# Kernel optimization log

Measured on AMD Instinct MI355X. Metric: run time of the kernel, lower is better.

The kernel has to match this reference:

```python
import jax, jax.numpy as jnp
import numpy as np


def _expand_chunk(x):
    # prepend the previous bucket along the chunk axis: [b, nb, bl, ...] -> [b, nb, 2*bl, ...]
    return jnp.concatenate([jnp.roll(x, 1, axis=1), x], axis=2)


def _gather_seq(origin, idx):
    # origin [b, s, d], idx [b, s, r] -> out[b, s, :, r] = origin[b, idx[b, s, r], :]
    b = origin.shape[0]
    g = origin[jnp.arange(b)[:, None, None], idx]  # [b, s, r, d]
    return jnp.transpose(g, (0, 1, 3, 2))          # [b, s, d, r]


def _count_dup_keys(inp, rounds):
    # inp [b, s, K] int32: count duplicate key indices within a window of `rounds` in sorted order
    sort_idx = jnp.argsort(inp, axis=2)
    sorted_k = jnp.take_along_axis(inp, sort_idx, axis=2)
    unsort = jnp.argsort(sort_idx, axis=2)
    cnt = jnp.ones(inp.shape, jnp.float32)
    for i in range(1, rounds):
        eq = (sorted_k[..., i:] == sorted_k[..., :-i]).astype(jnp.float32)
        pad = jnp.zeros(inp.shape[:-1] + (i,), jnp.float32)
        cnt = cnt + jnp.concatenate([pad, eq], axis=-1) + jnp.concatenate([eq, pad], axis=-1)
    return jnp.take_along_axis(cnt, unsort, axis=2)


def setup_inputs() -> dict:
    key = jax.random.key(0)
    k1, k2, k3 = jax.random.split(key, 3)
    B_M_H, SEQ, D_K, N_ROUNDS, N_BUCKETS = 32, 2048, 64, 4, 32
    query = jax.random.normal(k1, (B_M_H, SEQ, D_K), jnp.float32)
    value = jax.random.normal(k2, (B_M_H, SEQ, D_K), jnp.float32)
    rand_matrix = jax.random.normal(k3, (B_M_H, D_K, N_ROUNDS, N_BUCKETS // 2), jnp.float32)
    return {"query": query, "value": value, "rand_matrix": rand_matrix}


def reference(query, value, rand_matrix):
    b, s, d = query.shape
    nr = rand_matrix.shape[2]
    n_buckets = 2 * rand_matrix.shape[3]
    bl = s // n_buckets  # bucket_len

    # --- LSH hashing: argmax over [proj, -proj], then make hashes unique per position ---
    proj = jnp.einsum('bsd,bdrk->bsrk', query, rand_matrix)
    hashes = jnp.argmax(jnp.concatenate([proj, -proj], axis=-1), axis=-1).astype(jnp.int32)
    hashes = hashes * s + jnp.arange(s, dtype=jnp.int32)[None, :, None]  # [b, s, nr]

    sort_idx = jnp.argsort(hashes, axis=1)      # [b, s, nr]
    unsort_idx = jnp.argsort(sort_idx, axis=1)  # [b, s, nr]

    # --- sort queries into buckets ---
    q = _gather_seq(query, sort_idx).reshape(b, n_buckets, bl, d, nr)
    k = _expand_chunk(q)  # [b, nb, 2*bl, d, nr]
    k = k * jax.lax.rsqrt(jnp.maximum(jnp.sum(k * k, axis=-2, keepdims=True), 1e-12))

    qk = jnp.einsum('bnidr,bnjdr->bnijr', q, k) / np.float32(np.sqrt(d))  # [b, nb, bl, 2bl, nr]

    # --- causal / self masks on original positions ---
    qi = sort_idx.reshape(b, n_buckets, bl, nr) % s
    ki = _expand_chunk(qi)  # [b, nb, 2bl, nr]
    mask1 = (qi[:, :, :, None, :] < ki[:, :, None, :, :]).astype(jnp.float32)
    mask2 = (qi[:, :, :, None, :] == ki[:, :, None, :, :]).astype(jnp.float32)
    qk = qk * (1 - mask1) + mask1 * (-1e9)
    qk = qk * (1 - mask2) + mask2 * (-1e5)

    # --- duplicate-key counting across rounds ---
    ki_b = jnp.broadcast_to(ki[:, :, None, :, :], (b, n_buckets, bl, 2 * bl, nr)).reshape(b, s, 2 * bl * nr)
    count_keys = _count_dup_keys(ki_b, nr).reshape(b, s, 2 * bl, nr)

    qk = qk.reshape(b, s, 2 * bl, nr)
    lse = jax.scipy.special.logsumexp(qk, axis=2)  # [b, s, nr]
    sm = jnp.exp(qk - lse[:, :, None, :]) / count_keys

    v = _gather_seq(value, sort_idx).reshape(b, n_buckets, bl, d, nr)
    vk = _expand_chunk(v)  # [b, nb, 2bl, d, nr]
    sm = sm.reshape(b, n_buckets, bl, 2 * bl, nr)
    att = jnp.einsum('bnijr,bnjdr->bnidr', sm, vk).reshape(b, s, d, nr)

    # --- unsort back to original order, per round ---
    att = jnp.transpose(att, (0, 1, 3, 2))  # [b, s, nr, d]
    att = jnp.take_along_axis(att, jnp.broadcast_to(unsort_idx[:, :, :, None], att.shape), axis=1)
    lse = jnp.take_along_axis(lse, unsort_idx, axis=1)

    # --- combine rounds weighted by softmax of logsumexp ---
    w = jax.nn.softmax(lse, axis=-1)  # [b, s, nr]
    return jnp.einsum('bsrd,bsr->bsd', att, w)
```

## Files before the change

kernel.cpp:

```cpp
#include <hip/hip_runtime.h>

typedef unsigned short u16;
typedef unsigned int   u32;
typedef short bf16x8 __attribute__((ext_vector_type(8)));
typedef float f32x16 __attribute__((ext_vector_type(16)));

#define S_  2048
#define D_  64
#define NR_ 4
#define NB_ 32

#define AS 72
#define VS 136
#define PS 136

__device__ __forceinline__ float bf2f(u16 u){ return __uint_as_float(((u32)u)<<16); }
__device__ __forceinline__ u16 f2bf(float f){
  u32 u = __float_as_uint(f);
  u32 r = (u + 0x7fffu + ((u>>16)&1u)) >> 16;
  return (u16)r;
}
__device__ __forceinline__ u32 pk2bf(float a, float b){
#if __has_builtin(__builtin_amdgcn_cvt_pk_bf16_f32)
  auto r = __builtin_amdgcn_cvt_pk_bf16_f32(a, b);
  u32 u; __builtin_memcpy(&u, &r, 4); return u;
#else
  return (u32)f2bf(a) | ((u32)f2bf(b) << 16);
#endif
}
__device__ __forceinline__ u16 f2bf1(float a){ return (u16)pk2bf(a, a); }
__device__ __forceinline__ void unpack2(u32 w, float &a, float &b){
  a = __uint_as_float(w<<16);
  b = __uint_as_float(w & 0xffff0000u);
}
__device__ __forceinline__ bf16x8 ld8(const u16* p){
  union { uint4 u; bf16x8 v; } x;
  x.u = *(const uint4*)p;
  return x.v;
}

__global__ __launch_bounds__(128, 2) void k_hash(const float* __restrict__ q,
                                              const float* __restrict__ v,
                                              const float* __restrict__ R,
                                              int* __restrict__ hout,
                                              u16* __restrict__ qb,
                                              u16* __restrict__ vbuf,
                                              float* __restrict__ scq){
  __shared__ float Rl[4096];
  int b    = blockIdx.x >> 3;
  int pos0 = (blockIdx.x & 7) * 256 + threadIdx.x;
  int pos1 = pos0 + 128;

  {
    const float4* Rg = (const float4*)(R + (size_t)b * 4096);
    float4* Rs = (float4*)Rl;
    #pragma unroll
    for (int k = 0; k < 8; k++) Rs[k*128 + threadIdx.x] = Rg[k*128 + threadIdx.x];
  }
  __syncthreads();

  const float4* q40 = (const float4*)(q + ((size_t)b * S_ + pos0) * D_);
  const float4* q41 = (const float4*)(q + ((size_t)b * S_ + pos1) * D_);
  const float4* v40 = (const float4*)(v + ((size_t)b * S_ + pos0) * D_);
  const float4* v41 = (const float4*)(v + ((size_t)b * S_ + pos1) * D_);
  uint2* qw0 = (uint2*)(qb   + ((size_t)b * S_ + pos0) * D_);
  uint2* qw1 = (uint2*)(qb   + ((size_t)b * S_ + pos1) * D_);
  uint2* vw0 = (uint2*)(vbuf + ((size_t)b * S_ + pos0) * D_);
  uint2* vw1 = (uint2*)(vbuf + ((size_t)b * S_ + pos1) * D_);

  float acc0[64], acc1[64];
  #pragma unroll
  for (int i = 0; i < 64; i++){ acc0[i] = 0.f; acc1[i] = 0.f; }
  float ss0 = 0.f, ss1 = 0.f;

  #pragma unroll 4
  for (int c = 0; c < 16; c++){
    float4 wa = q40[c], wb = q41[c];
    float4 xa = v40[c], xb = v41[c];
    ss0 += wa.x*wa.x + wa.y*wa.y + wa.z*wa.z + wa.w*wa.w;
    ss1 += wb.x*wb.x + wb.y*wb.y + wb.z*wb.z + wb.w*wb.w;
    qw0[c] = make_uint2(pk2bf(wa.x, wa.y), pk2bf(wa.z, wa.w));
    qw1[c] = make_uint2(pk2bf(wb.x, wb.y), pk2bf(wb.z, wb.w));
    vw0[c] = make_uint2(pk2bf(xa.x, xa.y), pk2bf(xa.z, xa.w));
    vw1[c] = make_uint2(pk2bf(xb.x, xb.y), pk2bf(xb.z, xb.w));
    float qa[4] = {wa.x, wa.y, wa.z, wa.w};
    float qb_[4] = {wb.x, wb.y, wb.z, wb.w};
    #pragma unroll
    for (int dd = 0; dd < 4; dd++){
      int d = c * 4 + dd;
      const float4* Rr = (const float4*)(&Rl[d * 64]);
      #pragma unroll
      for (int k4 = 0; k4 < 16; k4++){
        float4 rv = Rr[k4];
        acc0[k4*4+0] += qa[dd] * rv.x;  acc1[k4*4+0] += qb_[dd] * rv.x;
        acc0[k4*4+1] += qa[dd] * rv.y;  acc1[k4*4+1] += qb_[dd] * rv.y;
        acc0[k4*4+2] += qa[dd] * rv.z;  acc1[k4*4+2] += qb_[dd] * rv.z;
        acc0[k4*4+3] += qa[dd] * rv.w;  acc1[k4*4+3] += qb_[dd] * rv.w;
      }
    }
  }
  scq[(size_t)b * S_ + pos0] = rsqrtf(fmaxf(ss0, 1e-12f)) * 0.125f;
  scq[(size_t)b * S_ + pos1] = rsqrtf(fmaxf(ss1, 1e-12f)) * 0.125f;

  #pragma unroll
  for (int r = 0; r < 4; r++){
    float bv0 = acc0[r*16]; int bi0 = 0;
    float bv1 = acc1[r*16]; int bi1 = 0;
    #pragma unroll
    for (int m = 1; m < 32; m++){
      float v0 = (m < 16) ? acc0[r*16 + m] : -acc0[r*16 + m - 16];
      float v1 = (m < 16) ? acc1[r*16 + m] : -acc1[r*16 + m - 16];
      if (v0 > bv0){ bv0 = v0; bi0 = m; }
      if (v1 > bv1){ bv1 = v1; bi1 = m; }
    }
    hout[((size_t)b * NR_ + r) * S_ + pos0] = bi0;
    hout[((size_t)b * NR_ + r) * S_ + pos1] = bi1;
  }
}

__global__ __launch_bounds__(256) void k_sort(const int* __restrict__ h,
                                              int* __restrict__ sidx,
                                              int* __restrict__ chk){
  __shared__ int cnt[32][257];
  __shared__ int base[32];
  int br = blockIdx.x;
  const int* hb = h + (size_t)br * S_;
  int t = threadIdx.x;

  #pragma unroll
  for (int hh = 0; hh < 32; hh++) cnt[hh][t] = 0;
  __syncthreads();

  int hv[8];
  const int4* hb4 = (const int4*)hb;
  int4 a0 = hb4[t*2], a1 = hb4[t*2+1];
  hv[0]=a0.x; hv[1]=a0.y; hv[2]=a0.z; hv[3]=a0.w;
  hv[4]=a1.x; hv[5]=a1.y; hv[6]=a1.z; hv[7]=a1.w;
  #pragma unroll
  for (int k = 0; k < 8; k++) cnt[hv[k]][t]++;
  __syncthreads();

  int wave = t >> 6, lane = t & 63;
  for (int hh = wave*8; hh < wave*8 + 8; hh++){
    int vals[4]; int s0 = 0;
    #pragma unroll
    for (int k = 0; k < 4; k++){ vals[k] = cnt[hh][lane*4+k]; s0 += vals[k]; }
    int incl = s0;
    #pragma unroll
    for (int off = 1; off < 64; off <<= 1){
      int o = __shfl_up(incl, off, 64);
      if (lane >= off) incl += o;
    }
    int run = incl - s0;
    #pragma unroll
    for (int k = 0; k < 4; k++){ int tmp = vals[k]; cnt[hh][lane*4+k] = run; run += tmp; }
    if (lane == 63) base[hh] = incl;
  }
  __syncthreads();
  if (t == 0){
    int run = 0;
    #pragma unroll
    for (int hh = 0; hh < 32; hh++){ int tot = base[hh]; base[hh] = run; run += tot; }
  }
  __syncthreads();

  int p0 = t * 8;
  #pragma unroll
  for (int k = 0; k < 8; k++){
    int hh = hv[k];
    int c = cnt[hh][t];
    int slot = base[hh] + c;
    cnt[hh][t] = c + 1;
    sidx[(size_t)br * S_ + slot]    = p0 + k;
    chk [(size_t)br * S_ + p0 + k]  = slot >> 6;
  }
}

__global__ __launch_bounds__(256, 4) void k_attn(const u16* __restrict__ qb,
                                                 const u16* __restrict__ vb,
                                                 const int* __restrict__ sidx,
                                                 const int* __restrict__ chk,
                                                 const float* __restrict__ scq,
                                                 float* __restrict__ lse_ws,
                                                 u16*  __restrict__ att_ws){
  __shared__ u16 A[128*AS];
  __shared__ u16 SM[64*PS];
  __shared__ int   pkey[128];
  __shared__ float rcnt[128];
  __shared__ float sc[128];

  int blk = blockIdx.x;
  int b = blk >> 7, r = (blk >> 5) & 3, n = blk & 31;
  int npv = (n + 31) & 31;
  int t = threadIdx.x;
  int lane = t & 63, w = t >> 6;
  const int* sb = sidx + ((size_t)b * NR_ + r) * S_;

  if (t < 128){
    int p = (t < 64) ? sb[npv*64 + t] : sb[n*64 + (t - 64)];
    pkey[t] = p;
    int c = 0;
    #pragma unroll
    for (int rr = 0; rr < 4; rr++){
      int ch = chk[((size_t)b * NR_ + rr) * S_ + p];
      c += (ch == n) || (ch == npv);
    }
    if (c < 1) c = 1;
    rcnt[t] = 1.0f / (float)c;
    sc[t] = scq[(size_t)b * S_ + p];
  }
  __syncthreads();

  {
    int row = t >> 1, half = t & 1;
    const uint4* src = (const uint4*)(qb + ((size_t)b*S_ + pkey[row])*D_) + half*4;
    uint4* dst = (uint4*)(&A[row*AS + half*32]);
    #pragma unroll
    for (int k = 0; k < 4; k++) dst[k] = src[k];
  }
  int jp = t & 63, dgrp = t >> 6;
  uint4 va0, va1, vb0, vb1;
  {
    const uint4* s0 = (const uint4*)(vb + ((size_t)b*S_ + pkey[2*jp  ])*D_ + dgrp*16);
    const uint4* s1 = (const uint4*)(vb + ((size_t)b*S_ + pkey[2*jp+1])*D_ + dgrp*16);
    va0 = s0[0]; va1 = s0[1]; vb0 = s1[0]; vb1 = s1[1];
  }
  __syncthreads();

  int Mt = w & 1, Nt0 = (w >> 1) * 2;
  f32x16 acc0, acc1;
  #pragma unroll
  for (int i = 0; i < 16; i++){ acc0[i] = 0.f; acc1[i] = 0.f; }
  {
    int mrow  = (64 + Mt*32 + (lane & 31)) * AS;
    int krow0 = (Nt0*32 + (lane & 31)) * AS;
    int krow1 = krow0 + 32*AS;
    int coff  = (lane >> 5) * 8;
    #pragma unroll
    for (int ks = 0; ks < 4; ks++){
      int o = ks*16 + coff;
      bf16x8 af = ld8(&A[mrow  + o]);
      bf16x8 b0 = ld8(&A[krow0 + o]);
      bf16x8 b1 = ld8(&A[krow1 + o]);
      acc0 = __builtin_amdgcn_mfma_f32_32x32x16_bf16(af, b0, acc0, 0, 0, 0);
      acc1 = __builtin_amdgcn_mfma_f32_32x32x16_bf16(af, b1, acc1, 0, 0, 0);
    }
  }
  {
    int h = lane >> 5;
    int pi[16];
    #pragma unroll
    for (int reg = 0; reg < 16; reg++){
      int il = (reg & 3) + 8*(reg >> 2) + 4*h;
      pi[reg] = pkey[64 + Mt*32 + il];
    }
    #pragma unroll
    for (int e = 0; e < 2; e++){
      int j = (Nt0 + e)*32 + (lane & 31);
      int pj = pkey[j];
      float scj = sc[j];
      #pragma unroll
      for (int reg = 0; reg < 16; reg++){
        int il = (reg & 3) + 8*(reg >> 2) + 4*h;
        float l = (e ? acc1[reg] : acc0[reg]) * scj;
        if (pi[reg] < pj)       l = -1000000000.0f;
        else if (pi[reg] == pj) l = -100000.0f;
        SM[(Mt*32 + il)*PS + j] = f2bf1(l);
      }
    }
  }
  __syncthreads();

  {
    int srow = t >> 2, seg = t & 3;
    uint4 u[4];
    const uint4* p4 = (const uint4*)(&SM[srow*PS + seg*32]);
    #pragma unroll
    for (int k = 0; k < 4; k++) u[k] = p4[k];
    float vals[32];
    #pragma unroll
    for (int k = 0; k < 4; k++){
      unpack2(u[k].x, vals[k*8+0], vals[k*8+1]);
      unpack2(u[k].y, vals[k*8+2], vals[k*8+3]);
      unpack2(u[k].z, vals[k*8+4], vals[k*8+5]);
      unpack2(u[k].w, vals[k*8+6], vals[k*8+7]);
    }
    float mx = -3.0e38f;
    #pragma unroll
    for (int k = 0; k < 32; k++) mx = fmaxf(mx, vals[k]);
    float sl = 0.f;
    #pragma unroll
    for (int k = 0; k < 32; k++){ vals[k] = __expf(vals[k] - mx); sl += vals[k]; }
    float mxg = fmaxf(mx, __shfl_xor(mx, 1, 64));
    mxg = fmaxf(mxg, __shfl_xor(mxg, 2, 64));
    float scale = __expf(mx - mxg);
    float s = sl * scale;
    s += __shfl_xor(s, 1, 64);
    s += __shfl_xor(s, 2, 64);
    float f = scale / s;
    const float4* rc4 = (const float4*)(&rcnt[seg*32]);
    u32 ob[16];
    #pragma unroll
    for (int k4 = 0; k4 < 8; k4++){
      float4 rc = rc4[k4];
      ob[k4*2+0] = pk2bf(vals[k4*4+0]*f*rc.x, vals[k4*4+1]*f*rc.y);
      ob[k4*2+1] = pk2bf(vals[k4*4+2]*f*rc.z, vals[k4*4+3]*f*rc.w);
    }
    uint4* d4 = (uint4*)(&SM[srow*PS + seg*32]);
    #pragma unroll
    for (int k = 0; k < 4; k++)
      d4[k] = make_uint4(ob[4*k], ob[4*k+1], ob[4*k+2], ob[4*k+3]);
    if (seg == 0)
      lse_ws[((size_t)b*S_ + pkey[64 + srow])*NR_ + r] = mxg + __logf(s);
  }

  {
    u32 au[8] = {va0.x, va0.y, va0.z, va0.w, va1.x, va1.y, va1.z, va1.w};
    u32 bu[8] = {vb0.x, vb0.y, vb0.z, vb0.w, vb1.x, vb1.y, vb1.z, vb1.w};
    u32* vtp = (u32*)A;
    #pragma unroll
    for (int k = 0; k < 8; k++){
      int d0 = dgrp*16 + 2*k;
      u32 even = (au[k] & 0xffffu) | (bu[k] << 16);
      u32 odd  = (au[k] >> 16)     | (bu[k] & 0xffff0000u);
      vtp[ d0      * (VS/2) + jp] = even;
      vtp[(d0 + 1) * (VS/2) + jp] = odd;
    }
  }
  __syncthreads();

  {
    int Mt2 = w >> 1, Nt2 = w & 1;
    f32x16 acc;
    #pragma unroll
    for (int i = 0; i < 16; i++) acc[i] = 0.f;
    int prow = (Mt2*32 + (lane & 31)) * PS;
    int vrow = (Nt2*32 + (lane & 31)) * VS;
    int coff = (lane >> 5) * 8;
    #pragma unroll
    for (int ks = 0; ks < 8; ks++){
      int o = ks*16 + coff;
      bf16x8 af = ld8(&SM[prow + o]);
      bf16x8 bf = ld8(&A[vrow + o]);
      acc = __builtin_amdgcn_mfma_f32_32x32x16_bf16(af, bf, acc, 0, 0, 0);
    }
    int h = lane >> 5;
    int dcol = Nt2*32 + (lane & 31);
    #pragma unroll
    for (int reg = 0; reg < 16; reg++){
      int il = (reg & 3) + 8*(reg >> 2) + 4*h;
      int p = pkey[64 + Mt2*32 + il];
      att_ws[(((size_t)b*S_ + p)*NR_ + r)*D_ + dcol] = f2bf1(acc[reg]);
    }
  }
}

__global__ __launch_bounds__(256) void k_comb(const float* __restrict__ lse_ws,
                                              const u16* __restrict__ att_ws,
                                              float* __restrict__ out){
  size_t idx4 = (size_t)blockIdx.x * 256 + threadIdx.x;
  size_t pd = idx4 >> 4;
  int d0 = (int)(idx4 & 15) * 4;
  float4 lv = *(const float4*)(lse_ws + pd * 4);
  float m = fmaxf(fmaxf(lv.x, lv.y), fmaxf(lv.z, lv.w));
  float e0 = __expf(lv.x - m), e1 = __expf(lv.y - m);
  float e2 = __expf(lv.z - m), e3 = __expf(lv.w - m);
  float inv = 1.0f / (e0 + e1 + e2 + e3);
  e0 *= inv; e1 *= inv; e2 *= inv; e3 *= inv;
  const u16* a = att_ws + pd * 256 + d0;
  uint2 u0 = *(const uint2*)(a);
  uint2 u1 = *(const uint2*)(a + 64);
  uint2 u2 = *(const uint2*)(a + 128);
  uint2 u3 = *(const uint2*)(a + 192);
  float4 o;
  float a0,b0,a1,b1,a2,b2,a3,b3;
  unpack2(u0.x,a0,b0); unpack2(u1.x,a1,b1); unpack2(u2.x,a2,b2); unpack2(u3.x,a3,b3);
  o.x = a0*e0 + a1*e1 + a2*e2 + a3*e3;
  o.y = b0*e0 + b1*e1 + b2*e2 + b3*e3;
  unpack2(u0.y,a0,b0); unpack2(u1.y,a1,b1); unpack2(u2.y,a2,b2); unpack2(u3.y,a3,b3);
  o.z = a0*e0 + a1*e1 + a2*e2 + a3*e3;
  o.w = b0*e0 + b1*e1 + b2*e2 + b3*e3;
  *(float4*)(out + pd * D_ + d0) = o;
}

extern "C" void kernel_launch(void* const* d_in, const int* in_sizes, int n_in,
                              void* d_out, int out_size, void* d_ws, size_t ws_size,
                              hipStream_t stream){
  const float* q = (const float*)d_in[0];
  const float* v = (const float*)d_in[1];
  const float* R = (const float*)d_in[2];

  char* w = (char*)d_ws;
  int*   h    = (int*)  (w + 0);
  int*   sidx = (int*)  (w + (size_t)(1u << 20));
  int*   chkA = (int*)  (w + (size_t)(2u << 20));
  float* lse  = (float*)(w + (size_t)(3u << 20));
  u16*   att  = (u16*)  (w + (size_t)(4u << 20));
  u16*   qb   = (u16*)  (w + (size_t)(36u << 20));
  u16*   vbuf = (u16*)  (w + (size_t)(44u << 20));
  float* scq  = (float*)(w + (size_t)(52u << 20));
  float* out  = (float*)d_out;

  k_hash <<<256,  128, 0, stream>>>(q, v, R, h, qb, vbuf, scq);
  k_sort <<<128,  256, 0, stream>>>(h, sidx, chkA);
  k_attn <<<4096, 256, 0, stream>>>(qb, vbuf, sidx, chkA, scq, lse, att);
  k_comb <<<4096, 256, 0, stream>>>(lse, att, out);
}
```

Baseline: 170.2 us.

## Transpose MFMA operands for packed stores; one position per hash thread

k_hash now runs 256 threads with one sequence position each instead of 128 threads with two, which cuts per-thread accumulator registers. In k_attn, both MFMA stages swap their A/B operands so each lane holds four consecutive columns. Score tiles can then be written to shared memory as packed 8-byte bf16 stores, and attention outputs go to global memory as packed uint2 stores instead of scattered 2-byte writes. The aim is fewer memory transactions and less register pressure, at the cost of a different LDS access pattern that may raise bank conflicts.

Result: faster. 150.7 us (-11.5%).

```diff
diff --git a/kernel.cpp b/kernel.cpp
--- a/kernel.cpp
+++ b/kernel.cpp
@@ -39,52 +39,43 @@
   return x.v;
 }
 
-__global__ __launch_bounds__(128, 2) void k_hash(const float* __restrict__ q,
-                                              const float* __restrict__ v,
-                                              const float* __restrict__ R,
-                                              int* __restrict__ hout,
-                                              u16* __restrict__ qb,
-                                              u16* __restrict__ vbuf,
-                                              float* __restrict__ scq){
+__global__ __launch_bounds__(256, 2) void k_hash(const float* __restrict__ q,
+                                                 const float* __restrict__ v,
+                                                 const float* __restrict__ R,
+                                                 int* __restrict__ hout,
+                                                 u16* __restrict__ qb,
+                                                 u16* __restrict__ vbuf,
+                                                 float* __restrict__ scq){
   __shared__ float Rl[4096];
-  int b    = blockIdx.x >> 3;
-  int pos0 = (blockIdx.x & 7) * 256 + threadIdx.x;
-  int pos1 = pos0 + 128;
+  int b   = blockIdx.x >> 3;
+  int pos = (blockIdx.x & 7) * 256 + threadIdx.x;
 
   {
     const float4* Rg = (const float4*)(R + (size_t)b * 4096);
     float4* Rs = (float4*)Rl;
     #pragma unroll
-    for (int k = 0; k < 8; k++) Rs[k*128 + threadIdx.x] = Rg[k*128 + threadIdx.x];
-  }
-  __syncthreads();
-
-  const float4* q40 = (const float4*)(q + ((size_t)b * S_ + pos0) * D_);
-  const float4* q41 = (const float4*)(q + ((size_t)b * S_ + pos1) * D_);
-  const float4* v40 = (const float4*)(v + ((size_t)b * S_ + pos0) * D_);
-  const float4* v41 = (const float4*)(v + ((size_t)b * S_ + pos1) * D_);
-  uint2* qw0 = (uint2*)(qb   + ((size_t)b * S_ + pos0) * D_);
-  uint2* qw1 = (uint2*)(qb   + ((size_t)b * S_ + pos1) * D_);
-  uint2* vw0 = (uint2*)(vbuf + ((size_t)b * S_ + pos0) * D_);
-  uint2* vw1 = (uint2*)(vbuf + ((size_t)b * S_ + pos1) * D_);
-
-  float acc0[64], acc1[64];
-  #pragma unroll
-  for (int i = 0; i < 64; i++){ acc0[i] = 0.f; acc1[i] = 0.f; }
-  float ss0 = 0.f, ss1 = 0.f;
+    for (int k = 0; k < 4; k++) Rs[k*256 + threadIdx.x] = Rg[k*256 + threadIdx.x];
+  }
+  __syncthreads();
+
+  const float4* q4 = (const float4*)(q + ((size_t)b * S_ + pos) * D_);
+  const float4* v4 = (const float4*)(v + ((size_t)b * S_ + pos) * D_);
+  uint2* qw = (uint2*)(qb   + ((size_t)b * S_ + pos) * D_);
+  uint2* vw = (uint2*)(vbuf + ((size_t)b * S_ + pos) * D_);
+
+  float acc[64];
+  #pragma unroll
+  for (int i = 0; i < 64; i++) acc[i] = 0.f;
+  float ss = 0.f;
 
   #pragma unroll 4
   for (int c = 0; c < 16; c++){
-    float4 wa = q40[c], wb = q41[c];
-    float4 xa = v40[c], xb = v41[c];
-    ss0 += wa.x*wa.x + wa.y*wa.y + wa.z*wa.z + wa.w*wa.w;
-    ss1 += wb.x*wb.x + wb.y*wb.y + wb.z*wb.z + wb.w*wb.w;
-    qw0[c] = make_uint2(pk2bf(wa.x, wa.y), pk2bf(wa.z, wa.w));
-    qw1[c] = make_uint2(pk2bf(wb.x, wb.y), pk2bf(wb.z, wb.w));
-    vw0[c] = make_uint2(pk2bf(xa.x, xa.y), pk2bf(xa.z, xa.w));
-    vw1[c] = make_uint2(pk2bf(xb.x, xb.y), pk2bf(xb.z, xb.w));
+    float4 wa = q4[c];
+    float4 xa = v4[c];
+    ss += wa.x*wa.x + wa.y*wa.y + wa.z*wa.z + wa.w*wa.w;
+    qw[c] = make_uint2(pk2bf(wa.x, wa.y), pk2bf(wa.z, wa.w));
+    vw[c] = make_uint2(pk2bf(xa.x, xa.y), pk2bf(xa.z, xa.w));
     float qa[4] = {wa.x, wa.y, wa.z, wa.w};
-    float qb_[4] = {wb.x, wb.y, wb.z, wb.w};
     #pragma unroll
     for (int dd = 0; dd < 4; dd++){
       int d = c * 4 + dd;
@@ -92,29 +83,24 @@
       #pragma unroll
       for (int k4 = 0; k4 < 16; k4++){
         float4 rv = Rr[k4];
-        acc0[k4*4+0] += qa[dd] * rv.x;  acc1[k4*4+0] += qb_[dd] * rv.x;
-        acc0[k4*4+1] += qa[dd] * rv.y;  acc1[k4*4+1] += qb_[dd] * rv.y;
-        acc0[k4*4+2] += qa[dd] * rv.z;  acc1[k4*4+2] += qb_[dd] * rv.z;
-        acc0[k4*4+3] += qa[dd] * rv.w;  acc1[k4*4+3] += qb_[dd] * rv.w;
+        acc[k4*4+0] += qa[dd] * rv.x;
+        acc[k4*4+1] += qa[dd] * rv.y;
+        acc[k4*4+2] += qa[dd] * rv.z;
+        acc[k4*4+3] += qa[dd] * rv.w;
       }
     }
   }
-  scq[(size_t)b * S_ + pos0] = rsqrtf(fmaxf(ss0, 1e-12f)) * 0.125f;
-  scq[(size_t)b * S_ + pos1] = rsqrtf(fmaxf(ss1, 1e-12f)) * 0.125f;
+  scq[(size_t)b * S_ + pos] = rsqrtf(fmaxf(ss, 1e-12f)) * 0.125f;
 
   #pragma unroll
   for (int r = 0; r < 4; r++){
-    float bv0 = acc0[r*16]; int bi0 = 0;
-    float bv1 = acc1[r*16]; int bi1 = 0;
+    float bv = acc[r*16]; int bi = 0;
     #pragma unroll
     for (int m = 1; m < 32; m++){
-      float v0 = (m < 16) ? acc0[r*16 + m] : -acc0[r*16 + m - 16];
-      float v1 = (m < 16) ? acc1[r*16 + m] : -acc1[r*16 + m - 16];
-      if (v0 > bv0){ bv0 = v0; bi0 = m; }
-      if (v1 > bv1){ bv1 = v1; bi1 = m; }
-    }
-    hout[((size_t)b * NR_ + r) * S_ + pos0] = bi0;
-    hout[((size_t)b * NR_ + r) * S_ + pos1] = bi1;
+      float vv = (m < 16) ? acc[r*16 + m] : -acc[r*16 + m - 16];
+      if (vv > bv){ bv = vv; bi = m; }
+    }
+    hout[((size_t)b * NR_ + r) * S_ + pos] = bi;
   }
 }
 
@@ -194,6 +180,8 @@
   int npv = (n + 31) & 31;
   int t = threadIdx.x;
   int lane = t & 63, w = t >> 6;
+  int la = lane & 31, hh = lane >> 5;
+  int coff = hh * 8;
   const int* sb = sidx + ((size_t)b * NR_ + r) * S_;
 
   if (t < 128){
@@ -227,45 +215,47 @@
   }
   __syncthreads();
 
-  int Mt = w & 1, Nt0 = (w >> 1) * 2;
-  f32x16 acc0, acc1;
-  #pragma unroll
-  for (int i = 0; i < 16; i++){ acc0[i] = 0.f; acc1[i] = 0.f; }
-  {
-    int mrow  = (64 + Mt*32 + (lane & 31)) * AS;
-    int krow0 = (Nt0*32 + (lane & 31)) * AS;
-    int krow1 = krow0 + 32*AS;
-    int coff  = (lane >> 5) * 8;
+  {
+    int jt = w;
+    f32x16 acc0, acc1;
+    #pragma unroll
+    for (int i = 0; i < 16; i++){ acc0[i] = 0.f; acc1[i] = 0.f; }
+    int arow  = (jt*32 + la) * AS;
+    int brow0 = (64 + la) * AS;
+    int brow1 = (96 + la) * AS;
     #pragma unroll
     for (int ks = 0; ks < 4; ks++){
       int o = ks*16 + coff;
-      bf16x8 af = ld8(&A[mrow  + o]);
-      bf16x8 b0 = ld8(&A[krow0 + o]);
-      bf16x8 b1 = ld8(&A[krow1 + o]);
+      bf16x8 af = ld8(&A[arow  + o]);
+      bf16x8 b0 = ld8(&A[brow0 + o]);
+      bf16x8 b1 = ld8(&A[brow1 + o]);
       acc0 = __builtin_amdgcn_mfma_f32_32x32x16_bf16(af, b0, acc0, 0, 0, 0);
       acc1 = __builtin_amdgcn_mfma_f32_32x32x16_bf16(af, b1, acc1, 0, 0, 0);
     }
-  }
-  {
-    int h = lane >> 5;
-    int pi[16];
-    #pragma unroll
-    for (int reg = 0; reg < 16; reg++){
-      int il = (reg & 3) + 8*(reg >> 2) + 4*h;
-      pi[reg] = pkey[64 + Mt*32 + il];
+    int pj[16]; float scj[16];
+    #pragma unroll
+    for (int g = 0; g < 4; g++){
+      int j0 = jt*32 + g*8 + 4*hh;
+      #pragma unroll
+      for (int m = 0; m < 4; m++){ pj[g*4+m] = pkey[j0+m]; scj[g*4+m] = sc[j0+m]; }
     }
     #pragma unroll
     for (int e = 0; e < 2; e++){
-      int j = (Nt0 + e)*32 + (lane & 31);
-      int pj = pkey[j];
-      float scj = sc[j];
+      int i = e*32 + la;
+      int pi = pkey[64 + i];
       #pragma unroll
-      for (int reg = 0; reg < 16; reg++){
-        int il = (reg & 3) + 8*(reg >> 2) + 4*h;
-        float l = (e ? acc1[reg] : acc0[reg]) * scj;
-        if (pi[reg] < pj)       l = -1000000000.0f;
-        else if (pi[reg] == pj) l = -100000.0f;
-        SM[(Mt*32 + il)*PS + j] = f2bf1(l);
+      for (int g = 0; g < 4; g++){
+        float l[4];
+        #pragma unroll
+        for (int m = 0; m < 4; m++){
+          int reg = g*4 + m;
+          float x = (e ? acc1[reg] : acc0[reg]) * scj[reg];
+          if (pi < pj[reg])       x = -1000000000.0f;
+          else if (pi == pj[reg]) x = -100000.0f;
+          l[m] = x;
+        }
+        int j0 = jt*32 + g*8 + 4*hh;
+        *(uint2*)(&SM[i*PS + j0]) = make_uint2(pk2bf(l[0], l[1]), pk2bf(l[2], l[3]));
       }
     }
   }
@@ -334,23 +324,23 @@
     f32x16 acc;
     #pragma unroll
     for (int i = 0; i < 16; i++) acc[i] = 0.f;
-    int prow = (Mt2*32 + (lane & 31)) * PS;
-    int vrow = (Nt2*32 + (lane & 31)) * VS;
-    int coff = (lane >> 5) * 8;
+    int arow = (Mt2*32 + la) * VS;
+    int brow = (Nt2*32 + la) * PS;
     #pragma unroll
     for (int ks = 0; ks < 8; ks++){
       int o = ks*16 + coff;
-      bf16x8 af = ld8(&SM[prow + o]);
-      bf16x8 bf = ld8(&A[vrow + o]);
+      bf16x8 af = ld8(&A[arow + o]);
+      bf16x8 bf = ld8(&SM[brow + o]);
       acc = __builtin_amdgcn_mfma_f32_32x32x16_bf16(af, bf, acc, 0, 0, 0);
     }
-    int h = lane >> 5;
-    int dcol = Nt2*32 + (lane & 31);
-    #pragma unroll
-    for (int reg = 0; reg < 16; reg++){
-      int il = (reg & 3) + 8*(reg >> 2) + 4*h;
-      int p = pkey[64 + Mt2*32 + il];
-      att_ws[(((size_t)b*S_ + p)*NR_ + r)*D_ + dcol] = f2bf1(acc[reg]);
+    int i = Nt2*32 + la;
+    int p = pkey[64 + i];
+    u16* base = att_ws + (((size_t)b*S_ + p)*NR_ + r)*D_ + Mt2*32 + 4*hh;
+    #pragma unroll
+    for (int g = 0; g < 4; g++){
+      uint2 val = make_uint2(pk2bf(acc[4*g+0], acc[4*g+1]),
+                             pk2bf(acc[4*g+2], acc[4*g+3]));
+      *(uint2*)(base + g*8) = val;
     }
   }
 }
@@ -401,7 +391,7 @@
   float* scq  = (float*)(w + (size_t)(52u << 20));
   float* out  = (float*)d_out;
 
-  k_hash <<<256,  128, 0, stream>>>(q, v, R, h, qb, vbuf, scq);
+  k_hash <<<256,  256, 0, stream>>>(q, v, R, h, qb, vbuf, scq);
   k_sort <<<128,  256, 0, stream>>>(h, sidx, chkA);
   k_attn <<<4096, 256, 0, stream>>>(qb, vbuf, sidx, chkA, scq, lse, att);
   k_comb <<<4096, 256, 0, stream>>>(lse, att, out);
```
